# Performance work log

Measured on AMD Instinct MI355X. Metric: run time of the kernel, lower is better.

The kernel has to match this reference:

```python
import jax, jax.numpy as jnp
import numpy as np


def setup_inputs() -> dict:
    key = jax.random.key(0)
    ks = jax.random.split(key, 6)
    B, L, D, H, U = 256, 225, 1280, 256, 256
    features = jax.random.normal(ks[0], (B, L, D), dtype=jnp.float32)
    hidden = jax.random.normal(ks[1], (B, H), dtype=jnp.float32)
    W1 = jax.random.normal(ks[2], (D, U), dtype=jnp.float32) * (1.0 / np.sqrt(D))
    b1 = jnp.zeros((U,), dtype=jnp.float32)
    W2 = jax.random.normal(ks[3], (H, U), dtype=jnp.float32) * (1.0 / np.sqrt(H))
    b2 = jnp.zeros((U,), dtype=jnp.float32)
    V = jax.random.normal(ks[4], (U, 1), dtype=jnp.float32) * (1.0 / np.sqrt(U))
    bV = jnp.zeros((1,), dtype=jnp.float32)
    return {"features": features, "hidden": hidden, "W1": W1, "b1": b1,
            "W2": W2, "b2": b2, "V": V, "bV": bV}


def reference(features, hidden, W1, b1, W2, b2, V, bV):
    # features: [B, L, D]; hidden: [B, H]
    proj_f = jnp.einsum('bld,du->blu', features, W1) + b1        # [B, L, U]
    proj_h = (hidden @ W2 + b2)[:, None, :]                      # [B, 1, U]
    score = jnp.tanh(proj_f + proj_h)                            # [B, L, U]
    logits = jnp.einsum('blu,uo->blo', score, V) + bV            # [B, L, 1]
    attn = jax.nn.softmax(logits, axis=1)                        # [B, L, 1]
    context = jnp.sum(attn * features, axis=1)                   # [B, D]
    return context
```

## Files before the change

### kernel.cpp

```cpp
#include <hip/hip_runtime.h>
#include <hip/hip_bf16.h>

#define B_ 256
#define L_ 225
#define D_ 1280
#define H_ 256
#define U_ 256

typedef __bf16  bf16x8 __attribute__((ext_vector_type(8)));
typedef float   f32x4  __attribute__((ext_vector_type(4)));
typedef unsigned short u16x8 __attribute__((ext_vector_type(8)));

__device__ __forceinline__ unsigned short f2bf(float f) {
    union { __hip_bfloat16 h; unsigned short u; } cv;
    cv.h = __float2bfloat16(f);
    return cv.u;
}

__device__ __forceinline__ void gload_lds16(const void* g, void* l) {
    __builtin_amdgcn_global_load_lds(
        (const __attribute__((address_space(1))) unsigned int*)g,
        (__attribute__((address_space(3))) unsigned int*)l,
        16, 0, 0);
}

__device__ __forceinline__ float wredsum(float x) {
#pragma unroll
    for (int off = 32; off > 0; off >>= 1) x += __shfl_xor(x, off, 64);
    return x;
}

__global__ void k_prep(const float* __restrict__ W1,
                       const float* __restrict__ hidden,
                       const float* __restrict__ W2,
                       const float* __restrict__ b1,
                       const float* __restrict__ b2,
                       __hip_bfloat16* __restrict__ w1t,
                       float* __restrict__ ph) {
    int bid = blockIdx.x;
    if (bid < 80) {
        __shared__ float tile[64][65];
        const int kt = bid >> 2;
        const int ut = bid & 3;
        const int k0 = kt * 64, u0 = ut * 64;
        const int w  = threadIdx.x >> 6;
        const int l  = threadIdx.x & 63;
#pragma unroll
        for (int i = 0; i < 16; ++i) {
            int row = w * 16 + i;
            tile[row][l] = W1[(size_t)(k0 + row) * U_ + u0 + l];
        }
        __syncthreads();
#pragma unroll
        for (int i = 0; i < 16; ++i) {
            int urow = w * 16 + i;
            w1t[(size_t)(u0 + urow) * D_ + k0 + l] = __float2bfloat16(tile[l][urow]);
        }
    } else {
        __shared__ float sh[H_];
        int b = bid - 80;
        int u = threadIdx.x;
        sh[u] = hidden[b * H_ + u];
        __syncthreads();
        float acc = b1[u] + b2[u];
#pragma unroll 8
        for (int h = 0; h < H_; ++h) acc += sh[h] * W2[h * U_ + u];
        ph[b * U_ + u] = acc;
    }
}

__global__ __launch_bounds__(1024, 4) void k_fused(
        const float* __restrict__ feat,
        const __hip_bfloat16* __restrict__ w1t,
        const float* __restrict__ ph,
        const float* __restrict__ Vv,
        float* __restrict__ out) {
    __shared__ __align__(128) char smem[138304];
    float* sV   = (float*)(smem + 131072);
    float* sPh  = (float*)(smem + 132096);
    float* sL   = (float*)(smem + 133120);
    float* sW   = (float*)(smem + 137216);
    float* sRed = (float*)(smem + 138240);

    const int tid  = threadIdx.x;
    const int lane = tid & 63;
    const int wave = tid >> 6;
    const int wr   = wave >> 2;
    const int wc   = wave & 3;
    const int b    = blockIdx.x;

    if (tid < 256) { sV[tid] = Vv[tid]; sPh[tid] = ph[b * 256 + tid]; }

    const int ar    = tid >> 2;
    const int arc   = ar < L_ ? ar : (L_ - 1);
    const int akseg = (tid & 3) << 4;
    const float* aSrc0 = feat + ((size_t)(b * L_ + arc) * D_ + akseg);
    const int ac80 = akseg >> 3;
    const int aswz = (ar & 7) << 4;

    f32x4 acc[4][4];
#pragma unroll
    for (int mi = 0; mi < 4; ++mi)
#pragma unroll
        for (int ni = 0; ni < 4; ++ni)
            acc[mi][ni] = (f32x4){0.f, 0.f, 0.f, 0.f};

    auto loadA = [&](int kt, f32x4* v) {
        const float* src = aSrc0 + kt * 64;
        v[0] = *reinterpret_cast<const f32x4*>(src);
        v[1] = *reinterpret_cast<const f32x4*>(src + 4);
        v[2] = *reinterpret_cast<const f32x4*>(src + 8);
        v[3] = *reinterpret_cast<const f32x4*>(src + 12);
    };
    auto stageB = [&](int kt, char* bufB) {
#pragma unroll
        for (int pass = 0; pass < 2; ++pass) {
            int s   = pass * 1024 + tid;
            int u   = s >> 3;
            int c8s = s & 7;
            int c8g = c8s ^ (u & 7);
            gload_lds16(w1t + (size_t)u * D_ + kt * 64 + c8g * 8, bufB + s * 16);
        }
    };
    auto storeA = [&](const f32x4* v, char* bufA) {
        u16x8 w0, w1;
        w0[0] = f2bf(v[0][0]); w0[1] = f2bf(v[0][1]); w0[2] = f2bf(v[0][2]); w0[3] = f2bf(v[0][3]);
        w0[4] = f2bf(v[1][0]); w0[5] = f2bf(v[1][1]); w0[6] = f2bf(v[1][2]); w0[7] = f2bf(v[1][3]);
        w1[0] = f2bf(v[2][0]); w1[1] = f2bf(v[2][1]); w1[2] = f2bf(v[2][2]); w1[3] = f2bf(v[2][3]);
        w1[4] = f2bf(v[3][0]); w1[5] = f2bf(v[3][1]); w1[6] = f2bf(v[3][2]); w1[7] = f2bf(v[3][3]);
        *reinterpret_cast<u16x8*>(bufA + (ar << 7) + ((ac80 << 4) ^ aswz))       = w0;
        *reinterpret_cast<u16x8*>(bufA + (ar << 7) + (((ac80 + 1) << 4) ^ aswz)) = w1;
    };
    auto compute = [&](const char* bufA, const char* bufB) {
#pragma unroll
        for (int ks = 0; ks < 2; ++ks) {
            const int kk2 = (ks * 32 + ((lane >> 4) << 3)) * 2;
            bf16x8 a[4], bb[4];
#pragma unroll
            for (int mi = 0; mi < 4; ++mi) {
                int r = wr * 64 + mi * 16 + (lane & 15);
                a[mi] = *reinterpret_cast<const bf16x8*>(bufA + (r << 7) + (kk2 ^ ((r & 7) << 4)));
            }
#pragma unroll
            for (int ni = 0; ni < 4; ++ni) {
                int u = wc * 64 + ni * 16 + (lane & 15);
                bb[ni] = *reinterpret_cast<const bf16x8*>(bufB + (u << 7) + (kk2 ^ ((u & 7) << 4)));
            }
#pragma unroll
            for (int mi = 0; mi < 4; ++mi)
#pragma unroll
                for (int ni = 0; ni < 4; ++ni)
                    acc[mi][ni] = __builtin_amdgcn_mfma_f32_16x16x32_bf16(
                        a[mi], bb[ni], acc[mi][ni], 0, 0, 0);
        }
    };

    {
        f32x4 v[4];
        loadA(0, v);
        stageB(0, smem + 32768);
        storeA(v, smem);
    }
    __syncthreads();
    int cur = 0;
    for (int kt = 0; kt < 20; ++kt) {
        char* bufN = smem + (cur ^ 1) * 65536;
        f32x4 v[4];
        if (kt < 19) { loadA(kt + 1, v); stageB(kt + 1, bufN + 32768); }
        char* bufC = smem + cur * 65536;
        compute(bufC, bufC + 32768);
        if (kt < 19) storeA(v, bufN);
        __syncthreads();
        cur ^= 1;
    }

    float phu[4], vu[4];
#pragma unroll
    for (int ni = 0; ni < 4; ++ni) {
        int u = wc * 64 + ni * 16 + (lane & 15);
        phu[ni] = sPh[u];
        vu[ni]  = sV[u];
    }
#pragma unroll
    for (int mi = 0; mi < 4; ++mi) {
#pragma unroll
        for (int rg = 0; rg < 4; ++rg) {
            int row = wr * 64 + mi * 16 + ((lane >> 4) << 2) + rg;
            float s = 0.f;
#pragma unroll
            for (int ni = 0; ni < 4; ++ni) {
                float x = acc[mi][ni][rg] + phu[ni];
                s += (1.f - 2.f / (__expf(2.f * x) + 1.f)) * vu[ni];
            }
            s += __shfl_xor(s, 1, 64);
            s += __shfl_xor(s, 2, 64);
            s += __shfl_xor(s, 4, 64);
            s += __shfl_xor(s, 8, 64);
            if ((lane & 15) == 0) sL[wc * 256 + row] = s;
        }
    }
    __syncthreads();
    float den_p = 0.f;
    if (tid < 256) {
        float lg = sL[tid] + sL[256 + tid] + sL[512 + tid] + sL[768 + tid];
        float w  = (tid < L_) ? __expf(lg) : 0.f;
        sW[tid] = w;
        den_p = w;
    }
    den_p = wredsum(den_p);
    if (lane == 0) sRed[wave] = den_p;
    __syncthreads();

    f32x4 c[5];
#pragma unroll
    for (int ch = 0; ch < 5; ++ch) c[ch] = (f32x4){0.f, 0.f, 0.f, 0.f};
    {
        const float* fB = feat + (size_t)b * L_ * D_ + (lane << 2);
        for (int l = wave; l < L_; l += 16) {
            float wa = sW[l];
            const float* ra = fB + (size_t)l * D_;
#pragma unroll
            for (int ch = 1; ch < 5; ++ch)
                c[ch] += wa * *reinterpret_cast<const f32x4*>(ra + ch * 256);
        }
        for (int l = wave; l < L_; l += 16) {
            c[0] += sW[l] * *reinterpret_cast<const f32x4*>(fB + (size_t)l * D_);
        }
    }

    float* pc = (float*)smem;
#pragma unroll
    for (int ch = 0; ch < 5; ++ch)
        *reinterpret_cast<f32x4*>(pc + wave * 1280 + ch * 256 + (lane << 2)) = c[ch];
    __syncthreads();
    if (tid < 320) {
        f32x4 s = (f32x4){0.f, 0.f, 0.f, 0.f};
#pragma unroll
        for (int w = 0; w < 16; ++w)
            s += *reinterpret_cast<const f32x4*>(pc + w * 1280 + (tid << 2));
        float den = 0.f;
#pragma unroll
        for (int i = 0; i < 16; ++i) den += sRed[i];
        s *= (1.f / den);
        *reinterpret_cast<f32x4*>(out + (size_t)b * D_ + (tid << 2)) = s;
    }
}

extern "C" void kernel_launch(void* const* d_in, const int* in_sizes, int n_in,
                              void* d_out, int out_size, void* d_ws, size_t ws_size,
                              hipStream_t stream) {
    const float* feat   = (const float*)d_in[0];
    const float* hidden = (const float*)d_in[1];
    const float* W1     = (const float*)d_in[2];
    const float* b1     = (const float*)d_in[3];
    const float* W2     = (const float*)d_in[4];
    const float* b2     = (const float*)d_in[5];
    const float* Vv     = (const float*)d_in[6];

    char* ws = (char*)d_ws;
    __hip_bfloat16* w1t = (__hip_bfloat16*)(ws);
    float* ph = (float*)(ws + 655360);
    float* out = (float*)d_out;

    k_prep <<<336, 256, 0, stream>>>(W1, hidden, W2, b1, b2, w1t, ph);
    k_fused<<<B_, 1024, 0, stream>>>(feat, w1t, ph, Vv, out);
}
```

Baseline: 126.8 us.

## Split each batch row across two blocks with single-buffered tiles and a combine kernel

The fused kernel now runs two 512-thread blocks per batch element, each covering about half of the sequence (113 or 112 rows) in a 128-row M tile. Each block writes an unnormalized partial context and a partial softmax denominator, and a new small kernel sums the two halves and normalizes. Shared memory drops from about 138 KB to about 54 KB by removing the double buffer, so more blocks can be resident per CU and the grid doubles to 512 blocks. In exchange, global-load latency is no longer overlapped with MFMA work inside a block, there is an extra launch, and the partial sums make a round trip through global memory. Softmax skips max subtraction in both versions, so combining the halves by plain addition matches the original unnormalized math.

```diff
diff --git a/kernel.cpp b/kernel.cpp
--- a/kernel.cpp
+++ b/kernel.cpp
@@ -6,6 +6,7 @@
 #define D_ 1280
 #define H_ 256
 #define U_ 256
+#define BM 128
 
 typedef __bf16  bf16x8 __attribute__((ext_vector_type(8)));
 typedef float   f32x4  __attribute__((ext_vector_type(4)));
@@ -69,32 +70,41 @@
     }
 }
 
-__global__ __launch_bounds__(1024, 4) void k_fused(
+__global__ __launch_bounds__(512, 4) void k_fused(
         const float* __restrict__ feat,
         const __hip_bfloat16* __restrict__ w1t,
         const float* __restrict__ ph,
         const float* __restrict__ Vv,
-        float* __restrict__ out) {
-    __shared__ __align__(128) char smem[138304];
-    float* sV   = (float*)(smem + 131072);
-    float* sPh  = (float*)(smem + 132096);
-    float* sL   = (float*)(smem + 133120);
-    float* sW   = (float*)(smem + 137216);
-    float* sRed = (float*)(smem + 138240);
+        float* __restrict__ num,
+        float* __restrict__ den) {
+    __shared__ __align__(128) char smem[53768];
+    char*  sA  = smem;
+    char*  sB  = smem + 16384;
+    float* sV  = (float*)(smem + 49152);
+    float* sPh = (float*)(smem + 50176);
+    float* sL  = (float*)(smem + 51200);
+    float* sW  = (float*)(smem + 53248);
+    float* sRed= (float*)(smem + 53760);
 
     const int tid  = threadIdx.x;
     const int lane = tid & 63;
     const int wave = tid >> 6;
     const int wr   = wave >> 2;
     const int wc   = wave & 3;
-    const int b    = blockIdx.x;
+    const int blk  = blockIdx.x;
+    const int b    = blk >> 1;
+    const int h    = blk & 1;
+    const int l0   = h * 113;
+    const int nl   = h ? 112 : 113;
 
     if (tid < 256) { sV[tid] = Vv[tid]; sPh[tid] = ph[b * 256 + tid]; }
 
+    const float* featH = feat + ((size_t)b * L_ + l0) * D_;
+
     const int ar    = tid >> 2;
-    const int arc   = ar < L_ ? ar : (L_ - 1);
+    const int arc   = ar < nl ? ar : (nl - 1);
     const int akseg = (tid & 3) << 4;
-    const float* aSrc0 = feat + ((size_t)(b * L_ + arc) * D_ + akseg);
+    const float* aSrc0 = featH + (size_t)arc * D_ + akseg;
     const int ac80 = akseg >> 3;
     const int aswz = (ar & 7) << 4;
 
@@ -105,33 +115,31 @@
         for (int ni = 0; ni < 4; ++ni)
             acc[mi][ni] = (f32x4){0.f, 0.f, 0.f, 0.f};
 
-    auto loadA = [&](int kt, f32x4* v) {
+    for (int kt = 0; kt < 20; ++kt) {
         const float* src = aSrc0 + kt * 64;
-        v[0] = *reinterpret_cast<const f32x4*>(src);
-        v[1] = *reinterpret_cast<const f32x4*>(src + 4);
-        v[2] = *reinterpret_cast<const f32x4*>(src + 8);
-        v[3] = *reinterpret_cast<const f32x4*>(src + 12);
-    };
-    auto stageB = [&](int kt, char* bufB) {
-#pragma unroll
-        for (int pass = 0; pass < 2; ++pass) {
-            int s   = pass * 1024 + tid;
-            int u   = s >> 3;
-            int c8s = s & 7;
-            int c8g = c8s ^ (u & 7);
-            gload_lds16(w1t + (size_t)u * D_ + kt * 64 + c8g * 8, bufB + s * 16);
-        }
-    };
-    auto storeA = [&](const f32x4* v, char* bufA) {
-        u16x8 w0, w1;
-        w0[0] = f2bf(v[0][0]); w0[1] = f2bf(v[0][1]); w0[2] = f2bf(v[0][2]); w0[3] = f2bf(v[0][3]);
-        w0[4] = f2bf(v[1][0]); w0[5] = f2bf(v[1][1]); w0[6] = f2bf(v[1][2]); w0[7] = f2bf(v[1][3]);
-        w1[0] = f2bf(v[2][0]); w1[1] = f2bf(v[2][1]); w1[2] = f2bf(v[2][2]); w1[3] = f2bf(v[2][3]);
-        w1[4] = f2bf(v[3][0]); w1[5] = f2bf(v[3][1]); w1[6] = f2bf(v[3][2]); w1[7] = f2bf(v[3][3]);
-        *reinterpret_cast<u16x8*>(bufA + (ar << 7) + ((ac80 << 4) ^ aswz))       = w0;
-        *reinterpret_cast<u16x8*>(bufA + (ar << 7) + (((ac80 + 1) << 4) ^ aswz)) = w1;
-    };
-    auto compute = [&](const char* bufA, const char* bufB) {
+        f32x4 v0 = *reinterpret_cast<const f32x4*>(src);
+        f32x4 v1 = *reinterpret_cast<const f32x4*>(src + 4);
+        f32x4 v2 = *reinterpret_cast<const f32x4*>(src + 8);
+        f32x4 v3 = *reinterpret_cast<const f32x4*>(src + 12);
+        __syncthreads();
+#pragma unroll
+        for (int p = 0; p < 4; ++p) {
+            int sI = p * 512 + tid;
+            int u  = sI >> 3;
+            int c8 = (sI & 7) ^ (u & 7);
+            gload_lds16(w1t + (size_t)u * D_ + kt * 64 + c8 * 8, sB + sI * 16);
+        }
+        {
+            u16x8 w0, w1;
+            w0[0] = f2bf(v0[0]); w0[1] = f2bf(v0[1]); w0[2] = f2bf(v0[2]); w0[3] = f2bf(v0[3]);
+            w0[4] = f2bf(v1[0]); w0[5] = f2bf(v1[1]); w0[6] = f2bf(v1[2]); w0[7] = f2bf(v1[3]);
+            w1[0] = f2bf(v2[0]); w1[1] = f2bf(v2[1]); w1[2] = f2bf(v2[2]); w1[3] = f2bf(v2[3]);
+            w1[4] = f2bf(v3[0]); w1[5] = f2bf(v3[1]); w1[6] = f2bf(v3[2]); w1[7] = f2bf(v3[3]);
+            *reinterpret_cast<u16x8*>(sA + (ar << 7) + ((ac80 << 4) ^ aswz))       = w0;
+            *reinterpret_cast<u16x8*>(sA + (ar << 7) + (((ac80 + 1) << 4) ^ aswz)) = w1;
+        }
+        __syncthreads();
+
 #pragma unroll
         for (int ks = 0; ks < 2; ++ks) {
             const int kk2 = (ks * 32 + ((lane >> 4) << 3)) * 2;
@@ -139,12 +147,12 @@
 #pragma unroll
             for (int mi = 0; mi < 4; ++mi) {
                 int r = wr * 64 + mi * 16 + (lane & 15);
-                a[mi] = *reinterpret_cast<const bf16x8*>(bufA + (r << 7) + (kk2 ^ ((r & 7) << 4)));
+                a[mi] = *reinterpret_cast<const bf16x8*>(sA + (r << 7) + (kk2 ^ ((r & 7) << 4)));
             }
 #pragma unroll
             for (int ni = 0; ni < 4; ++ni) {
                 int u = wc * 64 + ni * 16 + (lane & 15);
-                bb[ni] = *reinterpret_cast<const bf16x8*>(bufB + (u << 7) + (kk2 ^ ((u & 7) << 4)));
+                bb[ni] = *reinterpret_cast<const bf16x8*>(sB + (u << 7) + (kk2 ^ ((u & 7) << 4)));
             }
 #pragma unroll
             for (int mi = 0; mi < 4; ++mi)
@@ -153,26 +161,8 @@
                     acc[mi][ni] = __builtin_amdgcn_mfma_f32_16x16x32_bf16(
                         a[mi], bb[ni], acc[mi][ni], 0, 0, 0);
         }
-    };
-
-    {
-        f32x4 v[4];
-        loadA(0, v);
-        stageB(0, smem + 32768);
-        storeA(v, smem);
-    }
-    __syncthreads();
-    int cur = 0;
-    for (int kt = 0; kt < 20; ++kt) {
-        char* bufN = smem + (cur ^ 1) * 65536;
-        f32x4 v[4];
-        if (kt < 19) { loadA(kt + 1, v); stageB(kt + 1, bufN + 32768); }
-        char* bufC = smem + cur * 65536;
-        compute(bufC, bufC + 32768);
-        if (kt < 19) storeA(v, bufN);
-        __syncthreads();
-        cur ^= 1;
-    }
+    }
+    __syncthreads();
 
     float phu[4], vu[4];
 #pragma unroll
@@ -196,37 +186,36 @@
             s += __shfl_xor(s, 2, 64);
             s += __shfl_xor(s, 4, 64);
             s += __shfl_xor(s, 8, 64);
-            if ((lane & 15) == 0) sL[wc * 256 + row] = s;
-        }
-    }
-    __syncthreads();
-    float den_p = 0.f;
-    if (tid < 256) {
-        float lg = sL[tid] + sL[256 + tid] + sL[512 + tid] + sL[768 + tid];
-        float w  = (tid < L_) ? __expf(lg) : 0.f;
+            if ((lane & 15) == 0) sL[wc * 128 + row] = s;
+        }
+    }
+    __syncthreads();
+
+    if (tid < 128) {
+        float lg = sL[tid] + sL[128 + tid] + sL[256 + tid] + sL[384 + tid];
+        float w  = (tid < nl) ? __expf(lg) : 0.f;
         sW[tid] = w;
-        den_p = w;
-    }
-    den_p = wredsum(den_p);
-    if (lane == 0) sRed[wave] = den_p;
+        float d = wredsum(w);
+        if ((tid & 63) == 0) sRed[tid >> 6] = d;
+    }
     __syncthreads();
 
     f32x4 c[5];
 #pragma unroll
     for (int ch = 0; ch < 5; ++ch) c[ch] = (f32x4){0.f, 0.f, 0.f, 0.f};
     {
-        const float* fB = feat + (size_t)b * L_ * D_ + (lane << 2);
-        for (int l = wave; l < L_; l += 16) {
+        const float* fB = featH + (lane << 2);
+        for (int l = wave; l < nl; l += 8) {
             float wa = sW[l];
             const float* ra = fB + (size_t)l * D_;
 #pragma unroll
             for (int ch = 1; ch < 5; ++ch)
                 c[ch] += wa * *reinterpret_cast<const f32x4*>(ra + ch * 256);
         }
-        for (int l = wave; l < L_; l += 16) {
+        for (int l = wave; l < nl; l += 8)
             c[0] += sW[l] * *reinterpret_cast<const f32x4*>(fB + (size_t)l * D_);
-        }
-    }
+    }
+    __syncthreads();
 
     float* pc = (float*)smem;
 #pragma unroll
@@ -236,14 +225,21 @@
     if (tid < 320) {
         f32x4 s = (f32x4){0.f, 0.f, 0.f, 0.f};
 #pragma unroll
-        for (int w = 0; w < 16; ++w)
+        for (int w = 0; w < 8; ++w)
             s += *reinterpret_cast<const f32x4*>(pc + w * 1280 + (tid << 2));
-        float den = 0.f;
-#pragma unroll
-        for (int i = 0; i < 16; ++i) den += sRed[i];
-        s *= (1.f / den);
-        *reinterpret_cast<f32x4*>(out + (size_t)b * D_ + (tid << 2)) = s;
-    }
+        *reinterpret_cast<f32x4*>(num + (size_t)blk * 1280 + (tid << 2)) = s;
+    }
+    if (tid == 0) den[blk] = sRed[0] + sRed[1];
+}
+
+__global__ void k_out(const float* __restrict__ num, const float* __restrict__ den,
+                      float* __restrict__ out) {
+    int b = blockIdx.x;
+    int t = threadIdx.x;
+    f32x4 s = *reinterpret_cast<const f32x4*>(num + (size_t)(b * 2) * D_ + (t << 2))
+            + *reinterpret_cast<const f32x4*>(num + (size_t)(b * 2 + 1) * D_ + (t << 2));
+    s *= (1.f / (den[b * 2] + den[b * 2 + 1]));
+    *reinterpret_cast<f32x4*>(out + (size_t)b * D_ + (t << 2)) = s;
 }
 
 extern "C" void kernel_launch(void* const* d_in, const int* in_sizes, int n_in,
@@ -259,9 +255,12 @@
 
     char* ws = (char*)d_ws;
     __hip_bfloat16* w1t = (__hip_bfloat16*)(ws);
-    float* ph = (float*)(ws + 655360);
+    float* ph  = (float*)(ws + 655360);
+    float* num = (float*)(ws + 917504);
+    float* den = (float*)(ws + 3538944);
     float* out = (float*)d_out;
 
     k_prep <<<336, 256, 0, stream>>>(W1, hidden, W2, b1, b2, w1t, ph);
-    k_fused<<<B_, 1024, 0, stream>>>(feat, w1t, ph, Vv, out);
-}
+    k_fused<<<B_ * 2, 512, 0, stream>>>(feat, w1t, ph, Vv, num, den);
+    k_out  <<<B_, 320, 0, stream>>>(num, den, out);
+}
```

Result: faster. 123.4 us (-2.7%).
